# Performance work log

Hardware: AMD Instinct MI355X
Metric: run time of the kernel (lower is better)

## Reference

```python
import jax, jax.numpy as jnp
import numpy as np

N_NODES = 20000
N_EDGES = 320000
N_GRAPHS = 32
C = 256
L = 4
IN_DIM = 739
EDGE_DIM = 2 * C + 6
LN_EPS = 1e-5


def _layernorm(x, g, b):
    mu = jnp.mean(x, axis=-1, keepdims=True)
    var = jnp.mean(jnp.square(x - mu), axis=-1, keepdims=True)
    return (x - mu) * jax.lax.rsqrt(var + LN_EPS) * g + b


def setup_inputs() -> dict:
    key = jax.random.key(0)
    ks = jax.random.split(key, 20)
    d = {}
    d["x"] = jax.random.normal(ks[0], (N_NODES, IN_DIM), jnp.float32)
    d["x_pos"] = jax.random.normal(ks[1], (N_NODES, 3), jnp.float32)
    d["edge_index"] = jax.random.randint(ks[2], (2, N_EDGES), 0, N_NODES, jnp.int32)
    d["batch"] = jnp.sort(jax.random.randint(ks[3], (N_NODES,), 0, N_GRAPHS, jnp.int32))
    s = 0.02
    d["dense_w"] = jax.random.normal(ks[4], (IN_DIM, C), jnp.float32) * s
    d["dense_b"] = jnp.zeros((C,), jnp.float32)
    d["d1_w"] = jax.random.normal(ks[5], (L, C, C), jnp.float32) * s
    d["d1_b"] = jnp.zeros((L, C), jnp.float32)
    d["ln1_g"] = jnp.ones((L, EDGE_DIM), jnp.float32)
    d["ln1_b"] = jnp.zeros((L, EDGE_DIM), jnp.float32)
    d["w1_w"] = jax.random.normal(ks[6], (L, EDGE_DIM, 4), jnp.float32) * s
    d["w1_b"] = jnp.zeros((L, 4), jnp.float32)
    d["ln2_g"] = jnp.ones((L, 4), jnp.float32)
    d["ln2_b"] = jnp.zeros((L, 4), jnp.float32)
    d["w2_w"] = jax.random.normal(ks[7], (L, 4, 1), jnp.float32) * s
    d["w2_b"] = jnp.zeros((L, 1), jnp.float32)
    d["d2_w"] = jax.random.normal(ks[8], (L, C, C), jnp.float32) * s
    d["d2_b"] = jnp.zeros((L, C), jnp.float32)
    d["head_w"] = jax.random.normal(ks[9], (C, 1), jnp.float32) * s
    d["head_b"] = jnp.zeros((1,), jnp.float32)
    return d


def reference(x, x_pos, edge_index, batch, dense_w, dense_b, d1_w, d1_b,
              ln1_g, ln1_b, w1_w, w1_b, ln2_g, ln2_b, w2_w, w2_b,
              d2_w, d2_b, head_w, head_b):
    n = x.shape[0]
    src, dst = edge_index[0], edge_index[1]
    h = x @ dense_w + dense_b  # [N, C]
    for l in range(d1_w.shape[0]):
        # message: dense1 -> GELU (dropout is identity in eval)
        m = jax.nn.gelu(h @ d1_w[l] + d1_b[l], approximate=False)  # [N, C]
        sx = m[src]                                                # [E, C]
        # edge-MLP input: [src_x, dst_x, src_pos, dst_pos]
        e = jnp.concatenate([sx, m[dst], x_pos[src], x_pos[dst]], axis=-1)  # [E, 2C+6]
        e = _layernorm(e, ln1_g[l], ln1_b[l])
        e = jax.nn.gelu(e @ w1_w[l] + w1_b[l], approximate=False)  # [E, 4]
        e = _layernorm(e, ln2_g[l], ln2_b[l])
        w = jax.nn.sigmoid(e @ w2_w[l] + w2_b[l])                  # [E, 1]
        agg = jax.ops.segment_sum(sx * w, dst, num_segments=n)     # [N, C]
        # update: dense2 -> GELU
        h = jax.nn.gelu(agg @ d2_w[l] + d2_b[l], approximate=False)
    # global mean pool over graphs
    sums = jax.ops.segment_sum(h, batch, num_segments=N_GRAPHS)           # [G, C]
    cnts = jax.ops.segment_sum(jnp.ones((n, 1), h.dtype), batch, num_segments=N_GRAPHS)
    pooled = sums / jnp.maximum(cnts, 1.0)
    return pooled @ head_w + head_b  # [G, 1]
```

## Files before the change

### kernel.cpp

```cpp
#include <hip/hip_runtime.h>
#include <math.h>

#define N_NODES 20000
#define N_EDGES 320000
#define N_GRAPHS 32
#define CDIM 256
#define IN_DIMV 739
#define KPAD_DENSE 768
#define ED_DIM 518
#define NLAYERS 4
#define LN_EPS 1e-5f
#define SCAN_BLOCKS ((N_NODES + 255) / 256)

typedef _Float16 f16x8 __attribute__((ext_vector_type(8)));
typedef _Float16 f16x4 __attribute__((ext_vector_type(4)));
typedef float f32x4 __attribute__((ext_vector_type(4)));

__device__ __forceinline__ float gelu_exact(float x) {
    return 0.5f * x * (1.f + erff(x * 0.7071067811865475f));
}

__global__ __launch_bounds__(256)
void prep_all(const float* __restrict__ ln1_g, const float* __restrict__ ln1_b,
              const float* __restrict__ w1_w, float* __restrict__ cw,
              float* __restrict__ SgSb,
              const float* __restrict__ dense_w, _Float16* __restrict__ wt_dense,
              const float* __restrict__ d1_w, const float* __restrict__ d2_w,
              _Float16* __restrict__ wt_sq, int* __restrict__ deg,
              float* __restrict__ sdot) {
    __shared__ float smem[2048 + 64];
    int b = blockIdx.x, tid = threadIdx.x;
    if (b < 79) {
        int i = b * 256 + tid;
        if (i < N_NODES) deg[i] = 0;
    } else if (b < 83) {
        int l = b - 79;
        float sg[4] = {0, 0, 0, 0}, sb[4] = {0, 0, 0, 0};
        for (int i = tid; i < ED_DIM; i += 256) {
            float g = ln1_g[l * ED_DIM + i];
            float bb = ln1_b[l * ED_DIM + i];
            float4 w = *(const float4*)&w1_w[(size_t)(l * ED_DIM + i) * 4];
            float4 c = make_float4(g * w.x, g * w.y, g * w.z, g * w.w);
            *(float4*)&cw[(size_t)(l * ED_DIM + i) * 4] = c;
            sg[0] += c.x; sg[1] += c.y; sg[2] += c.z; sg[3] += c.w;
            sb[0] += bb * w.x; sb[1] += bb * w.y; sb[2] += bb * w.z; sb[3] += bb * w.w;
        }
        for (int c = 0; c < 4; c++) { smem[tid * 8 + c] = sg[c]; smem[tid * 8 + 4 + c] = sb[c]; }
        __syncthreads();
        for (int s = 128; s > 0; s >>= 1) {
            if (tid < s)
                for (int c = 0; c < 8; c++) smem[tid * 8 + c] += smem[(tid + s) * 8 + c];
            __syncthreads();
        }
        if (tid < 8) SgSb[l * 8 + tid] = smem[tid];
    } else if (b < 275) {
        int q = b - 83;
        int kt = q >> 3, nt = q & 7;
        int i = tid >> 5, j = tid & 31;
        float* T = smem;
#pragma unroll
        for (int ii = 0; ii < 4; ii++) {
            int k = kt * 32 + i + ii * 8;
            T[(i + ii * 8) * 33 + j] = (k < IN_DIMV) ? dense_w[(size_t)k * 256 + nt * 32 + j] : 0.f;
        }
        __syncthreads();
#pragma unroll
        for (int ii = 0; ii < 4; ii++) {
            int n = nt * 32 + i + ii * 8;
            wt_dense[(size_t)n * KPAD_DENSE + kt * 32 + j] = (_Float16)T[j * 33 + i + ii * 8];
        }
    } else if (b < 787) {
        int q = b - 275;
        int z = q >> 6, kt = (q >> 3) & 7, nt = q & 7;
        const float* W = (z < 4) ? d1_w + (size_t)z * 65536 : d2_w + (size_t)(z - 4) * 65536;
        _Float16* O = wt_sq + (size_t)z * 65536;
        int i = tid >> 5, j = tid & 31;
        float* T = smem;
#pragma unroll
        for (int ii = 0; ii < 4; ii++)
            T[(i + ii * 8) * 33 + j] = W[(size_t)(kt * 32 + i + ii * 8) * 256 + nt * 32 + j];
        __syncthreads();
#pragma unroll
        for (int ii = 0; ii < 4; ii++)
            O[(size_t)(nt * 32 + i + ii * 8) * 256 + kt * 32 + j] = (_Float16)T[j * 33 + i + ii * 8];
    } else {
        int i = (b - 787) * 256 + tid;
        if (i < N_NODES) sdot[i] = 0.f;
    }
}

__global__ void hist_gstart_kernel(const int* __restrict__ ei, const int* __restrict__ batch,
                                   int* __restrict__ deg, int* __restrict__ gstart) {
    int e = blockIdx.x * 256 + threadIdx.x;
    if (e < N_EDGES) atomicAdd(&deg[ei[N_EDGES + e]], 1);
    if (e < N_NODES) {
        int b = batch[e];
        int bprev = (e == 0) ? -1 : batch[e - 1];
        for (int g = bprev + 1; g <= b; g++) gstart[g] = e;
        if (e == N_NODES - 1)
            for (int g = b + 1; g <= N_GRAPHS; g++) gstart[g] = N_NODES;
    }
}

__global__ __launch_bounds__(256)
void scan1_kernel(const int* __restrict__ deg, int* __restrict__ bsum) {
    __shared__ int red[256];
    int t = threadIdx.x;
    int i = blockIdx.x * 256 + t;
    red[t] = (i < N_NODES) ? deg[i] : 0;
    __syncthreads();
    for (int s = 128; s > 0; s >>= 1) {
        if (t < s) red[t] += red[t + s];
        __syncthreads();
    }
    if (t == 0) bsum[blockIdx.x] = red[0];
}

__global__ __launch_bounds__(128)
void scan2_kernel(const int* __restrict__ bsum, int* __restrict__ boff) {
    __shared__ int s[128];
    int t = threadIdx.x;
    int v = (t < SCAN_BLOCKS) ? bsum[t] : 0;
    s[t] = v;
    __syncthreads();
    for (int off = 1; off < 128; off <<= 1) {
        int o = (t >= off) ? s[t - off] : 0;
        __syncthreads();
        s[t] += o;
        __syncthreads();
    }
    if (t < SCAN_BLOCKS) boff[t] = s[t] - v;
}

__global__ __launch_bounds__(256)
void scan3_kernel(const int* __restrict__ deg, const int* __restrict__ boff,
                  int* __restrict__ row_start, int* __restrict__ cursor) {
    __shared__ int s[256];
    int t = threadIdx.x;
    int i = blockIdx.x * 256 + t;
    int v = (i < N_NODES) ? deg[i] : 0;
    s[t] = v;
    __syncthreads();
    for (int off = 1; off < 256; off <<= 1) {
        int o = (t >= off) ? s[t - off] : 0;
        __syncthreads();
        s[t] += o;
        __syncthreads();
    }
    int base = boff[blockIdx.x];
    int excl = base + s[t] - v;
    if (i < N_NODES) {
        row_start[i] = excl;
        cursor[i] = excl;
    }
    if (i == N_NODES - 1) row_start[N_NODES] = base + s[t];
}

__global__ void scatter_kernel(const int* __restrict__ ei, int* __restrict__ cursor,
                               int* __restrict__ csr_src, int* __restrict__ slot) {
    int e = blockIdx.x * 256 + threadIdx.x;
    if (e < N_EDGES) {
        int d = ei[N_EDGES + e];
        int pos = atomicAdd(&cursor[d], 1);
        csr_src[pos] = ei[e];
        slot[e] = pos;
    }
}

__global__ __launch_bounds__(256)
void gemm_dense(const float* __restrict__ A, const _Float16* __restrict__ Bt,
                const float* __restrict__ bias, _Float16* __restrict__ C) {
    __shared__ __align__(16) _Float16 As[32 * 72];
    __shared__ __align__(16) _Float16 Bs[128 * 72];
    int tid = threadIdx.x;
    int row0 = blockIdx.x * 32;
    int col0 = blockIdx.y * 128;
    int wave = tid >> 6, lane = tid & 63;
    int quad = lane >> 4, lrow = lane & 15;
    int wrow = wave >> 1, wcol = wave & 1;

    int ar = tid >> 3, ak8 = (tid & 7) * 8;
    int br = tid >> 1, bh = (tid & 1) * 32;

    const float* Arow = &A[(size_t)(row0 + ar) * IN_DIMV];
    const _Float16* Brow = &Bt[(size_t)(col0 + br) * KPAD_DENSE];

    const int ntiles = KPAD_DENSE >> 6;
    float a_f[8];
#pragma unroll
    for (int j = 0; j < 8; j++) {
        int gk = ak8 + j;
        a_f[j] = (gk < IN_DIMV) ? Arow[gk] : 0.f;
    }
    uint4 b_raw0 = *(const uint4*)&Brow[bh];
    uint4 b_raw1 = *(const uint4*)&Brow[bh + 8];
    uint4 b_raw2 = *(const uint4*)&Brow[bh + 16];
    uint4 b_raw3 = *(const uint4*)&Brow[bh + 24];

    f32x4 acc[4];
#pragma unroll
    for (int t = 0; t < 4; t++) acc[t] = (f32x4){0.f, 0.f, 0.f, 0.f};

    for (int kt = 0; kt < ntiles; ++kt) {
        f16x8 ah;
#pragma unroll
        for (int j = 0; j < 8; j++) ah[j] = (_Float16)a_f[j];
        *(f16x8*)&As[ar * 72 + ak8] = ah;
        *(uint4*)&Bs[br * 72 + bh] = b_raw0;
        *(uint4*)&Bs[br * 72 + bh + 8] = b_raw1;
        *(uint4*)&Bs[br * 72 + bh + 16] = b_raw2;
        *(uint4*)&Bs[br * 72 + bh + 24] = b_raw3;
        __syncthreads();

        if (kt + 1 < ntiles) {
            int k0 = (kt + 1) << 6;
#pragma unroll
            for (int j = 0; j < 8; j++) {
                int gk = k0 + ak8 + j;
                a_f[j] = (gk < IN_DIMV) ? Arow[gk] : 0.f;
            }
            b_raw0 = *(const uint4*)&Brow[k0 + bh];
            b_raw1 = *(const uint4*)&Brow[k0 + bh + 8];
            b_raw2 = *(const uint4*)&Brow[k0 + bh + 16];
            b_raw3 = *(const uint4*)&Brow[k0 + bh + 24];
        }

#pragma unroll
        for (int h = 0; h < 2; h++) {
            f16x8 af = *(const f16x8*)&As[(wrow * 16 + lrow) * 72 + h * 32 + quad * 8];
#pragma unroll
            for (int t = 0; t < 4; t++) {
                f16x8 bf = *(const f16x8*)&Bs[((wcol * 4 + t) * 16 + lrow) * 72 + h * 32 + quad * 8];
                acc[t] = __builtin_amdgcn_mfma_f32_16x16x32_f16(af, bf, acc[t], 0, 0, 0);
            }
        }
        __syncthreads();
    }

    int orow = row0 + wrow * 16 + quad * 4;
#pragma unroll
    for (int t = 0; t < 4; t++) {
        int col = col0 + (wcol * 4 + t) * 16 + lrow;
        float bv = bias[col];
#pragma unroll
        for (int r = 0; r < 4; r++)
            C[(size_t)(orow + r) * 256 + col] = (_Float16)(acc[t][r] + bv);
    }
}

template <bool GELU, bool DOT>
__global__ __launch_bounds__(256)
void gemm_mfma(const _Float16* __restrict__ A, const _Float16* __restrict__ Bt,
               const float* __restrict__ bias, _Float16* __restrict__ C,
               const float* __restrict__ head_w, float* __restrict__ sdot) {
    __shared__ __align__(16) _Float16 As[32 * 72];
    __shared__ __align__(16) _Float16 Bs[128 * 72];
    int tid = threadIdx.x;
    int row0 = blockIdx.x * 32;
    int col0 = blockIdx.y * 128;
    int wave = tid >> 6, lane = tid & 63;
    int quad = lane >> 4, lrow = lane & 15;
    int wrow = wave >> 1, wcol = wave & 1;

    int ar = tid >> 3, ak8 = (tid & 7) * 8;
    int br = tid >> 1, bh = (tid & 1) * 32;

    const _Float16* Arow = &A[(size_t)(row0 + ar) * CDIM];
    const _Float16* Brow = &Bt[(size_t)(col0 + br) * CDIM];

    const int ntiles = CDIM >> 6;
    uint4 a_raw = *(const uint4*)&Arow[ak8];
    uint4 b_raw0 = *(const uint4*)&Brow[bh];
    uint4 b_raw1 = *(const uint4*)&Brow[bh + 8];
    uint4 b_raw2 = *(const uint4*)&Brow[bh + 16];
    uint4 b_raw3 = *(const uint4*)&Brow[bh + 24];

    f32x4 acc[4];
#pragma unroll
    for (int t = 0; t < 4; t++) acc[t] = (f32x4){0.f, 0.f, 0.f, 0.f};

    for (int kt = 0; kt < ntiles; ++kt) {
        *(uint4*)&As[ar * 72 + ak8] = a_raw;
        *(uint4*)&Bs[br * 72 + bh] = b_raw0;
        *(uint4*)&Bs[br * 72 + bh + 8] = b_raw1;
        *(uint4*)&Bs[br * 72 + bh + 16] = b_raw2;
        *(uint4*)&Bs[br * 72 + bh + 24] = b_raw3;
        __syncthreads();

        if (kt + 1 < ntiles) {
            int k0 = (kt + 1) << 6;
            a_raw = *(const uint4*)&Arow[k0 + ak8];
            b_raw0 = *(const uint4*)&Brow[k0 + bh];
            b_raw1 = *(const uint4*)&Brow[k0 + bh + 8];
            b_raw2 = *(const uint4*)&Brow[k0 + bh + 16];
            b_raw3 = *(const uint4*)&Brow[k0 + bh + 24];
        }

#pragma unroll
        for (int h = 0; h < 2; h++) {
            f16x8 af = *(const f16x8*)&As[(wrow * 16 + lrow) * 72 + h * 32 + quad * 8];
#pragma unroll
            for (int t = 0; t < 4; t++) {
                f16x8 bf = *(const f16x8*)&Bs[((wcol * 4 + t) * 16 + lrow) * 72 + h * 32 + quad * 8];
                acc[t] = __builtin_amdgcn_mfma_f32_16x16x32_f16(af, bf, acc[t], 0, 0, 0);
            }
        }
        __syncthreads();
    }

    int orow = row0 + wrow * 16 + quad * 4;
    if (DOT) {
        float dp[4] = {0.f, 0.f, 0.f, 0.f};
#pragma unroll
        for (int t = 0; t < 4; t++) {
            int col = col0 + (wcol * 4 + t) * 16 + lrow;
            float hw = head_w[col];
            float bv = bias[col];
#pragma unroll
            for (int r = 0; r < 4; r++)
                dp[r] += gelu_exact(acc[t][r] + bv) * hw;
        }
#pragma unroll
        for (int r = 0; r < 4; r++) {
#pragma unroll
            for (int off = 1; off < 16; off <<= 1)
                dp[r] += __shfl_xor(dp[r], off, 64);
        }
        if (lrow == 0) {
#pragma unroll
            for (int r = 0; r < 4; r++) atomicAdd(&sdot[orow + r], dp[r]);
        }
    } else {
#pragma unroll
        for (int t = 0; t < 4; t++) {
            int col = col0 + (wcol * 4 + t) * 16 + lrow;
            float bv = bias[col];
#pragma unroll
            for (int r = 0; r < 4; r++) {
                float v = acc[t][r] + bv;
                C[(size_t)(orow + r) * 256 + col] = (_Float16)(GELU ? gelu_exact(v) : v);
            }
        }
    }
}

__global__ __launch_bounds__(256)
void node_summary_kernel(const _Float16* __restrict__ m, const float* __restrict__ cw,
                         float* __restrict__ ns) {
    __shared__ __align__(16) float4 s_cw[512];
    int tid = threadIdx.x;
    for (int i = tid; i < 512; i += 256) s_cw[i] = *(const float4*)&cw[(size_t)i * 4];
    __syncthreads();
    int n = blockIdx.x * 4 + (tid >> 6);
    if (n >= N_NODES) return;
    int lane = tid & 63;
    f16x4 a4 = *(const f16x4*)&m[(size_t)n * CDIM + lane * 4];
    float av[4] = {(float)a4[0], (float)a4[1], (float)a4[2], (float)a4[3]};
    float Q1 = 0.f, Q2 = 0.f, P1[4] = {0, 0, 0, 0}, P2[4] = {0, 0, 0, 0};
#pragma unroll
    for (int j = 0; j < 4; j++) {
        Q1 += av[j];
        Q2 += av[j] * av[j];
        float4 c0 = s_cw[lane * 4 + j];
        float4 c1 = s_cw[256 + lane * 4 + j];
        P1[0] += av[j] * c0.x; P1[1] += av[j] * c0.y; P1[2] += av[j] * c0.z; P1[3] += av[j] * c0.w;
        P2[0] += av[j] * c1.x; P2[1] += av[j] * c1.y; P2[2] += av[j] * c1.z; P2[3] += av[j] * c1.w;
    }
#pragma unroll
    for (int off = 1; off < 64; off <<= 1) {
        Q1 += __shfl_xor(Q1, off, 64);
        Q2 += __shfl_xor(Q2, off, 64);
        P1[0] += __shfl_xor(P1[0], off, 64);
        P1[1] += __shfl_xor(P1[1], off, 64);
        P1[2] += __shfl_xor(P1[2], off, 64);
        P1[3] += __shfl_xor(P1[3], off, 64);
        P2[0] += __shfl_xor(P2[0], off, 64);
        P2[1] += __shfl_xor(P2[1], off, 64);
        P2[2] += __shfl_xor(P2[2], off, 64);
        P2[3] += __shfl_xor(P2[3], off, 64);
    }
    if (lane == 0) {
        float* p = &ns[(size_t)n * 12];
        *(float4*)p = make_float4(P1[0], P1[1], P1[2], P1[3]);
        *(float4*)(p + 4) = make_float4(P2[0], P2[1], P2[2], P2[3]);
        p[8] = Q1;
        p[9] = Q2;
    }
}

__global__ __launch_bounds__(256)
void edge_weight_kernel(const float* __restrict__ ns, const float* __restrict__ x_pos,
                        const int* __restrict__ ei, const float* __restrict__ cw,
                        const float* __restrict__ SgSb, const float* __restrict__ w1_b,
                        const float* __restrict__ ln2_g, const float* __restrict__ ln2_b,
                        const float* __restrict__ w2_w, const float* __restrict__ w2_b,
                        const int* __restrict__ slot, float* __restrict__ w_csr) {
    int e = blockIdx.x * 256 + threadIdx.x;
    if (e >= N_EDGES) return;
    int s = ei[e], d = ei[N_EDGES + e];
    const float* nss = &ns[(size_t)s * 12];
    const float* nsd = &ns[(size_t)d * 12];
    float4 p1 = *(const float4*)nss;
    float4 p2 = *(const float4*)(nsd + 4);
    float S1 = nss[8] + nsd[8];
    float S2 = nss[9] + nsd[9];
    float D[4] = {p1.x + p2.x, p1.y + p2.y, p1.z + p2.z, p1.w + p2.w};
    float ps[6];
    ps[0] = x_pos[(size_t)s * 3 + 0];
    ps[1] = x_pos[(size_t)s * 3 + 1];
    ps[2] = x_pos[(size_t)s * 3 + 2];
    ps[3] = x_pos[(size_t)d * 3 + 0];
    ps[4] = x_pos[(size_t)d * 3 + 1];
    ps[5] = x_pos[(size_t)d * 3 + 2];
#pragma unroll
    for (int k = 0; k < 6; k++) {
        S1 += ps[k];
        S2 += ps[k] * ps[k];
        float4 c = *(const float4*)&cw[(size_t)(512 + k) * 4];
        D[0] += ps[k] * c.x; D[1] += ps[k] * c.y; D[2] += ps[k] * c.z; D[3] += ps[k] * c.w;
    }
    const float inv = 1.f / 518.f;
    float mu = S1 * inv;
    float var = fmaf(-mu, mu, S2 * inv);
    float rstd = rsqrtf(var + LN_EPS);
    float t[4];
#pragma unroll
    for (int c = 0; c < 4; c++)
        t[c] = gelu_exact(rstd * (D[c] - mu * SgSb[c]) + SgSb[4 + c] + w1_b[c]);
    float mu2 = 0.25f * (t[0] + t[1] + t[2] + t[3]);
    float var2 = 0.25f * ((t[0] - mu2) * (t[0] - mu2) + (t[1] - mu2) * (t[1] - mu2) +
                          (t[2] - mu2) * (t[2] - mu2) + (t[3] - mu2) * (t[3] - mu2));
    float r2 = rsqrtf(var2 + LN_EPS);
    float z = w2_b[0];
#pragma unroll
    for (int c = 0; c < 4; c++)
        z += ((t[c] - mu2) * r2 * ln2_g[c] + ln2_b[c]) * w2_w[c];
    w_csr[slot[e]] = 1.f / (1.f + expf(-z));
}

__global__ __launch_bounds__(256)
void agg_kernel(const _Float16* __restrict__ m, const int* __restrict__ csr_src,
                const float* __restrict__ w_csr, const int* __restrict__ row_start,
                _Float16* __restrict__ agg) {
    int n = blockIdx.x * 4 + (threadIdx.x >> 6);
    if (n >= N_NODES) return;
    int lane = threadIdx.x & 63;
    int beg = row_start[n], end = row_start[n + 1];
    float a0 = 0.f, a1 = 0.f, a2 = 0.f, a3 = 0.f;
    int j = beg;
    for (; j + 8 <= end; j += 8) {
        int si[8];
        float wi[8];
#pragma unroll
        for (int u = 0; u < 8; u++) { si[u] = csr_src[j + u]; wi[u] = w_csr[j + u]; }
        f16x4 v[8];
#pragma unroll
        for (int u = 0; u < 8; u++) v[u] = *(const f16x4*)&m[(size_t)si[u] * CDIM + lane * 4];
#pragma unroll
        for (int u = 0; u < 8; u++) {
            a0 = fmaf(wi[u], (float)v[u][0], a0);
            a1 = fmaf(wi[u], (float)v[u][1], a1);
            a2 = fmaf(wi[u], (float)v[u][2], a2);
            a3 = fmaf(wi[u], (float)v[u][3], a3);
        }
    }
    for (; j < end; j++) {
        int s = csr_src[j];
        float w = w_csr[j];
        f16x4 v = *(const f16x4*)&m[(size_t)s * CDIM + lane * 4];
        a0 = fmaf(w, (float)v[0], a0);
        a1 = fmaf(w, (float)v[1], a1);
        a2 = fmaf(w, (float)v[2], a2);
        a3 = fmaf(w, (float)v[3], a3);
    }
    f16x4 o;
    o[0] = (_Float16)a0; o[1] = (_Float16)a1; o[2] = (_Float16)a2; o[3] = (_Float16)a3;
    *(f16x4*)&agg[(size_t)n * CDIM + lane * 4] = o;
}

__global__ __launch_bounds__(256)
void final_head_kernel(const float* __restrict__ sdot, const int* __restrict__ gstart,
                       const float* __restrict__ head_b, float* __restrict__ out) {
    int g = blockIdx.x;
    int t = threadIdx.x;
    int beg = gstart[g], end = gstart[g + 1];
    float s = 0.f;
    for (int i = beg + t; i < end; i += 256) s += sdot[i];
    __shared__ float red[256];
    red[t] = s;
    __syncthreads();
    for (int k = 128; k > 0; k >>= 1) {
        if (t < k) red[t] += red[t + k];
        __syncthreads();
    }
    if (t == 0) out[g] = red[0] / fmaxf((float)(end - beg), 1.f) + head_b[0];
}

extern "C" void kernel_launch(void* const* d_in, const int* in_sizes, int n_in,
                              void* d_out, int out_size, void* d_ws, size_t ws_size,
                              hipStream_t stream) {
    const float* x       = (const float*)d_in[0];
    const float* x_pos   = (const float*)d_in[1];
    const int*   ei      = (const int*)d_in[2];
    const int*   batch   = (const int*)d_in[3];
    const float* dense_w = (const float*)d_in[4];
    const float* dense_b = (const float*)d_in[5];
    const float* d1_w    = (const float*)d_in[6];
    const float* d1_b    = (const float*)d_in[7];
    const float* ln1_g   = (const float*)d_in[8];
    const float* ln1_b   = (const float*)d_in[9];
    const float* w1_w    = (const float*)d_in[10];
    const float* w1_b    = (const float*)d_in[11];
    const float* ln2_g   = (const float*)d_in[12];
    const float* ln2_b   = (const float*)d_in[13];
    const float* w2_w    = (const float*)d_in[14];
    const float* w2_b    = (const float*)d_in[15];
    const float* d2_w    = (const float*)d_in[16];
    const float* d2_b    = (const float*)d_in[17];
    const float* head_w  = (const float*)d_in[18];
    const float* head_b  = (const float*)d_in[19];
    float* out = (float*)d_out;

    _Float16* hbuf0 = (_Float16*)d_ws;
    _Float16* hbuf1 = hbuf0 + (size_t)N_NODES * CDIM;
    _Float16* wt_dense = hbuf1 + (size_t)N_NODES * CDIM;
    _Float16* wt_sq    = wt_dense + (size_t)256 * KPAD_DENSE;
    float* cw    = (float*)(wt_sq + (size_t)8 * 256 * 256);
    float* SgSb  = cw + (size_t)NLAYERS * ED_DIM * 4;
    float* ns    = SgSb + NLAYERS * 8;
    float* sdot  = ns + (size_t)N_NODES * 12;
    float* w_csr = sdot + N_NODES;
    int* gstart    = (int*)(w_csr + N_EDGES);
    int* deg       = gstart + N_GRAPHS + 1;
    int* row_start = deg + N_NODES;
    int* cursor    = row_start + N_NODES + 1;
    int* csr_src   = cursor + N_NODES;
    int* slot      = csr_src + N_EDGES;
    int* bsum      = slot + N_EDGES;
    int* boff      = bsum + SCAN_BLOCKS;

    prep_all<<<866, 256, 0, stream>>>(ln1_g, ln1_b, w1_w, cw, SgSb,
                                      dense_w, wt_dense, d1_w, d2_w, wt_sq, deg, sdot);

    hist_gstart_kernel<<<(N_EDGES + 255) / 256, 256, 0, stream>>>(ei, batch, deg, gstart);
    scan1_kernel<<<SCAN_BLOCKS, 256, 0, stream>>>(deg, bsum);
    scan2_kernel<<<1, 128, 0, stream>>>(bsum, boff);
    scan3_kernel<<<SCAN_BLOCKS, 256, 0, stream>>>(deg, boff, row_start, cursor);
    scatter_kernel<<<(N_EDGES + 255) / 256, 256, 0, stream>>>(ei, cursor, csr_src, slot);

    const dim3 GGRID(N_NODES / 32, 2);
    gemm_dense<<<GGRID, 256, 0, stream>>>(x, wt_dense, dense_b, hbuf0);

    _Float16* h = hbuf0;
    _Float16* other = hbuf1;
    for (int l = 0; l < NLAYERS; l++) {
        gemm_mfma<true, false><<<GGRID, 256, 0, stream>>>(
            h, wt_sq + (size_t)l * 65536, d1_b + l * CDIM, other, nullptr, nullptr);
        node_summary_kernel<<<(N_NODES + 3) / 4, 256, 0, stream>>>(
            other, cw + (size_t)l * ED_DIM * 4, ns);
        edge_weight_kernel<<<(N_EDGES + 255) / 256, 256, 0, stream>>>(
            ns, x_pos, ei, cw + (size_t)l * ED_DIM * 4, SgSb + l * 8, w1_b + l * 4,
            ln2_g + l * 4, ln2_b + l * 4, w2_w + l * 4, w2_b + l, slot, w_csr);
        agg_kernel<<<(N_NODES + 3) / 4, 256, 0, stream>>>(other, csr_src, w_csr, row_start, h);
        if (l < NLAYERS - 1) {
            gemm_mfma<true, false><<<GGRID, 256, 0, stream>>>(
                h, wt_sq + (size_t)(4 + l) * 65536, d2_b + l * CDIM, other, nullptr, nullptr);
        } else {
            gemm_mfma<true, true><<<GGRID, 256, 0, stream>>>(
                h, wt_sq + (size_t)(4 + l) * 65536, d2_b + l * CDIM, other, head_w, sdot);
        }
        _Float16* tmp = h; h = other; other = tmp;
    }

    final_head_kernel<<<N_GRAPHS, 256, 0, stream>>>(sdot, gstart, head_b, out);
}
```

Before: 529.3 us.

## Fuse node-summary reduction into dense1 GEMM epilogue and coalesce dense A loads

Removes the separate node_summary kernel by computing the per-node LayerNorm statistics and the projections onto the folded edge-MLP weights in the epilogue of the dense1 GEMM. Partial sums are reduced across lanes and accumulated into ns with atomics, so ns must be zeroed beforehand: in prep_all for the first layer and inside agg_kernel for later layers. This saves a kernel launch and one re-read of the message tensor per layer, at the cost of many float atomics and higher register pressure in the epilogue. It also rewrites the input GEMM's A loads so that each lane reads consecutive columns across rows, which gives coalesced fp32 reads of the 739-wide x.

```diff
diff --git a/kernel.cpp b/kernel.cpp
--- a/kernel.cpp
+++ b/kernel.cpp
@@ -27,7 +27,7 @@
               const float* __restrict__ dense_w, _Float16* __restrict__ wt_dense,
               const float* __restrict__ d1_w, const float* __restrict__ d2_w,
               _Float16* __restrict__ wt_sq, int* __restrict__ deg,
-              float* __restrict__ sdot) {
+              float* __restrict__ sdot, float* __restrict__ ns) {
     __shared__ float smem[2048 + 64];
     int b = blockIdx.x, tid = threadIdx.x;
     if (b < 79) {
@@ -83,9 +83,12 @@
 #pragma unroll
         for (int ii = 0; ii < 4; ii++)
             O[(size_t)(nt * 32 + i + ii * 8) * 256 + kt * 32 + j] = (_Float16)T[j * 33 + i + ii * 8];
-    } else {
+    } else if (b < 866) {
         int i = (b - 787) * 256 + tid;
         if (i < N_NODES) sdot[i] = 0.f;
+    } else {
+        int i = (b - 866) * 256 + tid;
+        if (i < N_NODES * 12) ns[i] = 0.f;
     }
 }
 
@@ -179,18 +182,15 @@
     int quad = lane >> 4, lrow = lane & 15;
     int wrow = wave >> 1, wcol = wave & 1;
 
-    int ar = tid >> 3, ak8 = (tid & 7) * 8;
     int br = tid >> 1, bh = (tid & 1) * 32;
-
-    const float* Arow = &A[(size_t)(row0 + ar) * IN_DIMV];
     const _Float16* Brow = &Bt[(size_t)(col0 + br) * KPAD_DENSE];
 
     const int ntiles = KPAD_DENSE >> 6;
     float a_f[8];
 #pragma unroll
-    for (int j = 0; j < 8; j++) {
-        int gk = ak8 + j;
-        a_f[j] = (gk < IN_DIMV) ? Arow[gk] : 0.f;
+    for (int i = 0; i < 8; i++) {
+        int gk = lane;
+        a_f[i] = (gk < IN_DIMV) ? A[(size_t)(row0 + wave + i * 4) * IN_DIMV + gk] : 0.f;
     }
     uint4 b_raw0 = *(const uint4*)&Brow[bh];
     uint4 b_raw1 = *(const uint4*)&Brow[bh + 8];
@@ -202,10 +202,9 @@
     for (int t = 0; t < 4; t++) acc[t] = (f32x4){0.f, 0.f, 0.f, 0.f};
 
     for (int kt = 0; kt < ntiles; ++kt) {
-        f16x8 ah;
-#pragma unroll
-        for (int j = 0; j < 8; j++) ah[j] = (_Float16)a_f[j];
-        *(f16x8*)&As[ar * 72 + ak8] = ah;
+#pragma unroll
+        for (int i = 0; i < 8; i++)
+            As[(wave + i * 4) * 72 + lane] = (_Float16)a_f[i];
         *(uint4*)&Bs[br * 72 + bh] = b_raw0;
         *(uint4*)&Bs[br * 72 + bh + 8] = b_raw1;
         *(uint4*)&Bs[br * 72 + bh + 16] = b_raw2;
@@ -214,11 +213,11 @@
 
         if (kt + 1 < ntiles) {
             int k0 = (kt + 1) << 6;
-#pragma unroll
-            for (int j = 0; j < 8; j++) {
-                int gk = k0 + ak8 + j;
-                a_f[j] = (gk < IN_DIMV) ? Arow[gk] : 0.f;
-            }
+            int gk = k0 + lane;
+            bool ok = gk < IN_DIMV;
+#pragma unroll
+            for (int i = 0; i < 8; i++)
+                a_f[i] = ok ? A[(size_t)(row0 + wave + i * 4) * IN_DIMV + gk] : 0.f;
             b_raw0 = *(const uint4*)&Brow[k0 + bh];
             b_raw1 = *(const uint4*)&Brow[k0 + bh + 8];
             b_raw2 = *(const uint4*)&Brow[k0 + bh + 16];
@@ -248,11 +247,11 @@
     }
 }
 
-template <bool GELU, bool DOT>
+template <int MODE>
 __global__ __launch_bounds__(256)
 void gemm_mfma(const _Float16* __restrict__ A, const _Float16* __restrict__ Bt,
                const float* __restrict__ bias, _Float16* __restrict__ C,
-               const float* __restrict__ head_w, float* __restrict__ sdot) {
+               const float* __restrict__ aux, float* __restrict__ outv) {
     __shared__ __align__(16) _Float16 As[32 * 72];
     __shared__ __align__(16) _Float16 Bs[128 * 72];
     int tid = threadIdx.x;
@@ -309,12 +308,12 @@
     }
 
     int orow = row0 + wrow * 16 + quad * 4;
-    if (DOT) {
+    if (MODE == 2) {
         float dp[4] = {0.f, 0.f, 0.f, 0.f};
 #pragma unroll
         for (int t = 0; t < 4; t++) {
             int col = col0 + (wcol * 4 + t) * 16 + lrow;
-            float hw = head_w[col];
+            float hw = aux[col];
             float bv = bias[col];
 #pragma unroll
             for (int r = 0; r < 4; r++)
@@ -328,63 +327,68 @@
         }
         if (lrow == 0) {
 #pragma unroll
-            for (int r = 0; r < 4; r++) atomicAdd(&sdot[orow + r], dp[r]);
-        }
-    } else {
+            for (int r = 0; r < 4; r++) atomicAdd(&outv[orow + r], dp[r]);
+        }
+    } else if (MODE == 1) {
+        float p1[4][4], p2[4][4], q1[4], q2[4];
+#pragma unroll
+        for (int r = 0; r < 4; r++) {
+            q1[r] = 0.f; q2[r] = 0.f;
+#pragma unroll
+            for (int c = 0; c < 4; c++) { p1[r][c] = 0.f; p2[r][c] = 0.f; }
+        }
 #pragma unroll
         for (int t = 0; t < 4; t++) {
             int col = col0 + (wcol * 4 + t) * 16 + lrow;
             float bv = bias[col];
+            float4 c0 = *(const float4*)&aux[(size_t)col * 4];
+            float4 c1 = *(const float4*)&aux[(size_t)(256 + col) * 4];
 #pragma unroll
             for (int r = 0; r < 4; r++) {
-                float v = acc[t][r] + bv;
-                C[(size_t)(orow + r) * 256 + col] = (_Float16)(GELU ? gelu_exact(v) : v);
+                float v = gelu_exact(acc[t][r] + bv);
+                C[(size_t)(orow + r) * 256 + col] = (_Float16)v;
+                q1[r] += v; q2[r] += v * v;
+                p1[r][0] += v * c0.x; p1[r][1] += v * c0.y;
+                p1[r][2] += v * c0.z; p1[r][3] += v * c0.w;
+                p2[r][0] += v * c1.x; p2[r][1] += v * c1.y;
+                p2[r][2] += v * c1.z; p2[r][3] += v * c1.w;
             }
         }
-    }
-}
-
-__global__ __launch_bounds__(256)
-void node_summary_kernel(const _Float16* __restrict__ m, const float* __restrict__ cw,
-                         float* __restrict__ ns) {
-    __shared__ __align__(16) float4 s_cw[512];
-    int tid = threadIdx.x;
-    for (int i = tid; i < 512; i += 256) s_cw[i] = *(const float4*)&cw[(size_t)i * 4];
-    __syncthreads();
-    int n = blockIdx.x * 4 + (tid >> 6);
-    if (n >= N_NODES) return;
-    int lane = tid & 63;
-    f16x4 a4 = *(const f16x4*)&m[(size_t)n * CDIM + lane * 4];
-    float av[4] = {(float)a4[0], (float)a4[1], (float)a4[2], (float)a4[3]};
-    float Q1 = 0.f, Q2 = 0.f, P1[4] = {0, 0, 0, 0}, P2[4] = {0, 0, 0, 0};
-#pragma unroll
-    for (int j = 0; j < 4; j++) {
-        Q1 += av[j];
-        Q2 += av[j] * av[j];
-        float4 c0 = s_cw[lane * 4 + j];
-        float4 c1 = s_cw[256 + lane * 4 + j];
-        P1[0] += av[j] * c0.x; P1[1] += av[j] * c0.y; P1[2] += av[j] * c0.z; P1[3] += av[j] * c0.w;
-        P2[0] += av[j] * c1.x; P2[1] += av[j] * c1.y; P2[2] += av[j] * c1.z; P2[3] += av[j] * c1.w;
-    }
-#pragma unroll
-    for (int off = 1; off < 64; off <<= 1) {
-        Q1 += __shfl_xor(Q1, off, 64);
-        Q2 += __shfl_xor(Q2, off, 64);
-        P1[0] += __shfl_xor(P1[0], off, 64);
-        P1[1] += __shfl_xor(P1[1], off, 64);
-        P1[2] += __shfl_xor(P1[2], off, 64);
-        P1[3] += __shfl_xor(P1[3], off, 64);
-        P2[0] += __shfl_xor(P2[0], off, 64);
-        P2[1] += __shfl_xor(P2[1], off, 64);
-        P2[2] += __shfl_xor(P2[2], off, 64);
-        P2[3] += __shfl_xor(P2[3], off, 64);
-    }
-    if (lane == 0) {
-        float* p = &ns[(size_t)n * 12];
-        *(float4*)p = make_float4(P1[0], P1[1], P1[2], P1[3]);
-        *(float4*)(p + 4) = make_float4(P2[0], P2[1], P2[2], P2[3]);
-        p[8] = Q1;
-        p[9] = Q2;
+#pragma unroll
+        for (int off = 1; off < 16; off <<= 1) {
+#pragma unroll
+            for (int r = 0; r < 4; r++) {
+                q1[r] += __shfl_xor(q1[r], off, 64);
+                q2[r] += __shfl_xor(q2[r], off, 64);
+#pragma unroll
+                for (int c = 0; c < 4; c++) {
+                    p1[r][c] += __shfl_xor(p1[r][c], off, 64);
+                    p2[r][c] += __shfl_xor(p2[r][c], off, 64);
+                }
+            }
+        }
+        if (lrow == 0) {
+#pragma unroll
+            for (int r = 0; r < 4; r++) {
+                float* p = &outv[(size_t)(orow + r) * 12];
+#pragma unroll
+                for (int c = 0; c < 4; c++) {
+                    atomicAdd(p + c, p1[r][c]);
+                    atomicAdd(p + 4 + c, p2[r][c]);
+                }
+                atomicAdd(p + 8, q1[r]);
+                atomicAdd(p + 9, q2[r]);
+            }
+        }
+    } else {
+#pragma unroll
+        for (int t = 0; t < 4; t++) {
+            int col = col0 + (wcol * 4 + t) * 16 + lrow;
+            float bv = bias[col];
+#pragma unroll
+            for (int r = 0; r < 4; r++)
+                C[(size_t)(orow + r) * 256 + col] = (_Float16)gelu_exact(acc[t][r] + bv);
+        }
     }
 }
 
@@ -441,7 +445,7 @@
 __global__ __launch_bounds__(256)
 void agg_kernel(const _Float16* __restrict__ m, const int* __restrict__ csr_src,
                 const float* __restrict__ w_csr, const int* __restrict__ row_start,
-                _Float16* __restrict__ agg) {
+                _Float16* __restrict__ agg, float* __restrict__ ns) {
     int n = blockIdx.x * 4 + (threadIdx.x >> 6);
     if (n >= N_NODES) return;
     int lane = threadIdx.x & 63;
@@ -476,6 +480,7 @@
     f16x4 o;
     o[0] = (_Float16)a0; o[1] = (_Float16)a1; o[2] = (_Float16)a2; o[3] = (_Float16)a3;
     *(f16x4*)&agg[(size_t)n * CDIM + lane * 4] = o;
+    if (lane < 12) ns[(size_t)n * 12 + lane] = 0.f;
 }
 
 __global__ __launch_bounds__(256)
@@ -539,8 +544,8 @@
     int* bsum      = slot + N_EDGES;
     int* boff      = bsum + SCAN_BLOCKS;
 
-    prep_all<<<866, 256, 0, stream>>>(ln1_g, ln1_b, w1_w, cw, SgSb,
-                                      dense_w, wt_dense, d1_w, d2_w, wt_sq, deg, sdot);
+    prep_all<<<1804, 256, 0, stream>>>(ln1_g, ln1_b, w1_w, cw, SgSb,
+                                       dense_w, wt_dense, d1_w, d2_w, wt_sq, deg, sdot, ns);
 
     hist_gstart_kernel<<<(N_EDGES + 255) / 256, 256, 0, stream>>>(ei, batch, deg, gstart);
     scan1_kernel<<<SCAN_BLOCKS, 256, 0, stream>>>(deg, bsum);
@@ -554,19 +559,19 @@
     _Float16* h = hbuf0;
     _Float16* other = hbuf1;
     for (int l = 0; l < NLAYERS; l++) {
-        gemm_mfma<true, false><<<GGRID, 256, 0, stream>>>(
-            h, wt_sq + (size_t)l * 65536, d1_b + l * CDIM, other, nullptr, nullptr);
-        node_summary_kernel<<<(N_NODES + 3) / 4, 256, 0, stream>>>(
-            other, cw + (size_t)l * ED_DIM * 4, ns);
+        gemm_mfma<1><<<GGRID, 256, 0, stream>>>(
+            h, wt_sq + (size_t)l * 65536, d1_b + l * CDIM, other,
+            cw + (size_t)l * ED_DIM * 4, ns);
         edge_weight_kernel<<<(N_EDGES + 255) / 256, 256, 0, stream>>>(
             ns, x_pos, ei, cw + (size_t)l * ED_DIM * 4, SgSb + l * 8, w1_b + l * 4,
             ln2_g + l * 4, ln2_b + l * 4, w2_w + l * 4, w2_b + l, slot, w_csr);
-        agg_kernel<<<(N_NODES + 3) / 4, 256, 0, stream>>>(other, csr_src, w_csr, row_start, h);
+        agg_kernel<<<(N_NODES + 3) / 4, 256, 0, stream>>>(other, csr_src, w_csr, row_start,
+                                                          h, ns);
         if (l < NLAYERS - 1) {
-            gemm_mfma<true, false><<<GGRID, 256, 0, stream>>>(
+            gemm_mfma<0><<<GGRID, 256, 0, stream>>>(
                 h, wt_sq + (size_t)(4 + l) * 65536, d2_b + l * CDIM, other, nullptr, nullptr);
         } else {
-            gemm_mfma<true, true><<<GGRID, 256, 0, stream>>>(
+            gemm_mfma<2><<<GGRID, 256, 0, stream>>>(
                 h, wt_sq + (size_t)(4 + l) * 65536, d2_b + l * CDIM, other, head_w, sdot);
         }
         _Float16* tmp = h; h = other; other = tmp;
```

New measurement: 627.6 us. 18.6% more time.
